# Kernel tuning notes

Measured on AMD Instinct MI355X. Metric: run time of the kernel, lower is better.

## Reference

```python
import jax, jax.numpy as jnp
import numpy as np

V = 6890          # SMPL vertex count
RAYS, POINTS = 256, 64
LATENT_DIM = 16
RES_HI, RES_LO = 10, 4


def posenc(x, res):
    # NeRF-style encoding: [x, sin(2^k x), cos(2^k x)] for k in 0..res-1 -> D*(1+2*res)
    freqs = 2.0 ** jnp.arange(res, dtype=x.dtype)            # [res]
    xf = x[..., None, :] * freqs[:, None]                    # [..., res, D]
    n = x.shape[:-1]
    s = jnp.sin(xf).reshape(*n, -1)
    c = jnp.cos(xf).reshape(*n, -1)
    return jnp.concatenate([x, s, c], axis=-1)


def setup_inputs() -> dict:
    key = jax.random.key(0)
    ks = jax.random.split(key, 12)
    inp = {}
    inp['pts'] = jax.random.normal(ks[0], (RAYS, POINTS, 6), jnp.float32)
    inp['keypoints'] = jax.random.normal(ks[1], (V, 3), jnp.float32)
    # invertible per-vertex 4x4 transforms: identity + small noise, stored [4,4,V]
    noise = 0.1 * jax.random.normal(ks[2], (4, 4, V), jnp.float32)
    inp['trans_kp'] = jnp.eye(4, dtype=jnp.float32)[:, :, None] + noise
    inp['neighbors'] = jax.random.randint(ks[3], (V, 7), 0, V, jnp.int32)
    inp['rest_pose'] = jax.random.normal(ks[4], (V, 3), jnp.float32)
    inp['latent'] = jax.random.normal(ks[5], (V, LATENT_DIM), jnp.float32)
    d_in = 7 * ((2 * RES_HI + 1) * 4 + LATENT_DIM)  # 700
    inp['W1'] = 0.05 * jax.random.normal(ks[6], (d_in, 256), jnp.float32)
    inp['b1'] = jnp.zeros((256,), jnp.float32)
    inp['W2'] = 0.05 * jax.random.normal(ks[7], (256, 256), jnp.float32)
    inp['b2'] = jnp.zeros((256,), jnp.float32)
    inp['W3'] = 0.05 * jax.random.normal(ks[8], (256, 256), jnp.float32)
    inp['b3'] = jnp.zeros((256,), jnp.float32)
    return inp


def reference(pts, keypoints, trans_kp, neighbors, rest_pose, latent,
              W1, b1, W2, b2, W3, b3):
    rays, points, _ = pts.shape
    p, view_dir = jnp.split(pts, 2, axis=-1)
    p = p.reshape(rays * points, 3)                          # [N,3]

    # brute-force 1-NN of p into keypoints
    d2 = ((p * p).sum(-1, keepdims=True)
          - 2.0 * p @ keypoints.T
          + (keypoints * keypoints).sum(-1))                 # [N,V]
    knn_index = jnp.argmin(d2, axis=1)                       # [N]

    # inverse transforms, keep rotation part: [3,3,V]
    T = jnp.linalg.inv(jnp.transpose(trans_kp, (2, 0, 1)))   # [V,4,4]
    R = jnp.transpose(T, (1, 2, 0))[:3, :3]                  # [3,3,V]

    vidx = neighbors[knn_index]                              # [N,7]
    vdist = p[:, None, :] - keypoints[vidx]                  # [N,7,3]

    diff = p - keypoints[knn_index]                          # [N,3]
    Rg = R[:, :, knn_index]                                  # [3,3,N]
    direction = jnp.einsum('ijn,nj->ni', Rg, diff)           # [N,3]
    nrm = jnp.linalg.norm(direction, axis=-1, keepdims=True)
    direction = direction / jnp.maximum(nrm, 1e-12)

    vfeat = jnp.concatenate(
        [rest_pose[vidx].reshape(-1, 21),
         jnp.linalg.norm(vdist, axis=-1)], axis=-1)          # [N,28]
    lfeat = latent[vidx].reshape(-1, 7 * latent.shape[1])    # [N,112]

    h = jnp.concatenate([posenc(vfeat, RES_HI), lfeat], -1)  # [N,700]
    h = jax.nn.relu(h @ W1 + b1)
    h = jax.nn.relu(h @ W2 + b2)
    h = h @ W3 + b3                                          # [N,256]

    out = jnp.concatenate([h, posenc(direction, RES_LO)], -1)  # [N,283]
    return out.reshape(rays, points, -1)
```

## Files before the change

### kernel.cpp

```cpp
#include <hip/hip_runtime.h>
#include <hip/hip_bf16.h>
#include <math.h>

#define V_N   6890
#define N_PTS 16384
#define D_IN  700
#define D_INP 704
#define D_HID 256
#define D_OUT 283
#define NCHUNK 32
#define CHUNK  216
#define GAP_EPS 1e-4f

#define RINV4_OFF 0
#define KP4_OFF   82688
#define RP4_OFF   110272
#define PB4_OFF   170640
#define WT1_OFF   2267792
#define WT2_OFF   2357904
#define WT3_OFF   2390672
#define X_OFF     2423440

typedef __attribute__((ext_vector_type(8))) short short8;
typedef __attribute__((ext_vector_type(4))) float f32x4;

__device__ __forceinline__ unsigned short f2bf(float f) {
    unsigned int u = __builtin_bit_cast(unsigned int, f);
    u += 0x7fffu + ((u >> 16) & 1u);
    return (unsigned short)(u >> 16);
}

__device__ __forceinline__ float fsin(float x) {
    return __builtin_amdgcn_sinf(__builtin_amdgcn_fractf(x * 0.15915494309189535f));
}
__device__ __forceinline__ float fcos(float x) {
    return __builtin_amdgcn_cosf(__builtin_amdgcn_fractf(x * 0.15915494309189535f));
}

__device__ __forceinline__ void glds16(const void* g, void* l) {
    __builtin_amdgcn_global_load_lds(
        (const __attribute__((address_space(1))) void*)g,
        (__attribute__((address_space(3))) void*)l, 16, 0, 0);
}

__device__ __forceinline__ int swzoff(int r, int sub) {
    return ((r << 2) | (sub ^ ((r >> 1) & 3))) << 4;
}

#define SCAN_BLOCKS 2048
#define PREP_BLOCKS 27
__global__ __launch_bounds__(256) void prep_scan_kernel(
    const float* __restrict__ pts, const float* __restrict__ keyp,
    const float* __restrict__ trans, const float* __restrict__ restp,
    const float* __restrict__ W1, const float* __restrict__ W2,
    const float* __restrict__ W3,
    float4* __restrict__ rinv4, float4* __restrict__ kp4, float4* __restrict__ rp4,
    unsigned short* __restrict__ wt1, unsigned short* __restrict__ wt2,
    unsigned short* __restrict__ wt3, float4* __restrict__ pb4)
{
    __shared__ float4 s_kp[CHUNK];
    int bx = blockIdx.x, tid = threadIdx.x;

    if (bx < SCAN_BLOCKS) {
        int c = bx >> 6;
        int n = (bx & 63) * 256 + tid;
        int v0 = c * CHUNK;
        int nv = min(V_N - v0, CHUNK);
        if (tid < nv) {
            int v = v0 + tid;
            float kx = keyp[v*3+0], ky = keyp[v*3+1], kz = keyp[v*3+2];
            s_kp[tid] = make_float4(kx, ky, kz, kx*kx + ky*ky + kz*kz);
        }
        __syncthreads();

        float px2 = 2.0f * pts[n*6+0], py2 = 2.0f * pts[n*6+1], pz2 = 2.0f * pts[n*6+2];
        float m1 = 1e30f, m2 = 1e30f;
        int bi = 0x7fffffff;

#define KNN_STEP(kk, jj)                                            \
    {                                                               \
        float d = kk.w - (px2*kk.x + py2*kk.y + pz2*kk.z);          \
        bool lt = d < m1;                                           \
        m2 = lt ? m1 : fminf(m2, d);                                \
        bi = lt ? (jj) : bi;                                        \
        m1 = fminf(m1, d);                                          \
    }
        int j = 0;
        for (; j + 4 <= nv; j += 4) {
            float4 k0 = s_kp[j], k1 = s_kp[j+1], k2 = s_kp[j+2], k3 = s_kp[j+3];
            KNN_STEP(k0, v0+j); KNN_STEP(k1, v0+j+1);
            KNN_STEP(k2, v0+j+2); KNN_STEP(k3, v0+j+3);
        }
        for (; j < nv; ++j) {
            float4 k0 = s_kp[j];
            KNN_STEP(k0, v0+j);
        }
#undef KNN_STEP
        pb4[(size_t)c*N_PTS + n] = make_float4(m1, m2, __int_as_float(bi), 0.0f);

    } else if (bx < SCAN_BLOCKS + PREP_BLOCKS) {
        int v = (bx - SCAN_BLOCKS) * 256 + tid;
        if (v >= V_N) return;
        float m[16];
#pragma unroll
        for (int i = 0; i < 16; ++i) m[i] = trans[i * V_N + v];

        float i0  =  m[5]*m[10]*m[15] - m[5]*m[11]*m[14] - m[9]*m[6]*m[15] + m[9]*m[7]*m[14] + m[13]*m[6]*m[11] - m[13]*m[7]*m[10];
        float i4  = -m[4]*m[10]*m[15] + m[4]*m[11]*m[14] + m[8]*m[6]*m[15] - m[8]*m[7]*m[14] - m[12]*m[6]*m[11] + m[12]*m[7]*m[10];
        float i8  =  m[4]*m[9]*m[15]  - m[4]*m[11]*m[13] - m[8]*m[5]*m[15] + m[8]*m[7]*m[13] + m[12]*m[5]*m[11] - m[12]*m[7]*m[9];
        float i12 = -m[4]*m[9]*m[14]  + m[4]*m[10]*m[13] + m[8]*m[5]*m[14] - m[8]*m[6]*m[13] - m[12]*m[5]*m[10] + m[12]*m[6]*m[9];
        float i1  = -m[1]*m[10]*m[15] + m[1]*m[11]*m[14] + m[9]*m[2]*m[15] - m[9]*m[3]*m[14] - m[13]*m[2]*m[11] + m[13]*m[3]*m[10];
        float i5  =  m[0]*m[10]*m[15] - m[0]*m[11]*m[14] - m[8]*m[2]*m[15] + m[8]*m[3]*m[14] + m[12]*m[2]*m[11] - m[12]*m[3]*m[10];
        float i9  = -m[0]*m[9]*m[15]  + m[0]*m[11]*m[13] + m[8]*m[1]*m[15] - m[8]*m[3]*m[13] - m[12]*m[1]*m[11] + m[12]*m[3]*m[9];
        float i2  =  m[1]*m[6]*m[15]  - m[1]*m[7]*m[14]  - m[5]*m[2]*m[15] + m[5]*m[3]*m[14] + m[13]*m[2]*m[7]  - m[13]*m[3]*m[6];
        float i6  = -m[0]*m[6]*m[15]  + m[0]*m[7]*m[14]  + m[4]*m[2]*m[15] - m[4]*m[3]*m[14] - m[12]*m[2]*m[7]  + m[12]*m[3]*m[6];
        float i10 =  m[0]*m[5]*m[15]  - m[0]*m[7]*m[13]  - m[4]*m[1]*m[15] + m[4]*m[3]*m[13] + m[12]*m[1]*m[7]  - m[12]*m[3]*m[5];

        float det = m[0]*i0 + m[1]*i4 + m[2]*i8 + m[3]*i12;
        float id = 1.0f / det;
        rinv4[v*3+0] = make_float4(i0*id, i1*id, i2*id, i4*id);
        rinv4[v*3+1] = make_float4(i5*id, i6*id, i8*id, i9*id);
        rinv4[v*3+2] = make_float4(i10*id, 0.0f, 0.0f, 0.0f);

        float kx = keyp[v*3], ky = keyp[v*3+1], kz = keyp[v*3+2];
        kp4[v] = make_float4(kx, ky, kz, kx*kx + ky*ky + kz*kz);
        rp4[v] = make_float4(restp[v*3], restp[v*3+1], restp[v*3+2], 0.0f);
    } else {
        int idx = (bx - SCAN_BLOCKS - PREP_BLOCKS) * 256 + tid;
        const int N1 = 256 * D_INP;
        const int N2 = 256 * 256;
        if (idx < N1) {
            int n = idx / D_INP, k = idx - n * D_INP;
            float v = (k < D_IN) ? W1[k * 256 + n] : 0.0f;
            wt1[n * D_INP + k] = f2bf(v);
        } else if (idx < N1 + N2) {
            int t = idx - N1;
            int n = t >> 8, k = t & 255;
            wt2[n * 256 + k] = f2bf(W2[k * 256 + n]);
        } else if (idx < N1 + 2 * N2) {
            int t = idx - N1 - N2;
            int n = t >> 8, k = t & 255;
            wt3[n * 256 + k] = f2bf(W3[k * 256 + n]);
        }
    }
}

__global__ __launch_bounds__(256) void feat_kernel(
    const float* __restrict__ pts, const int* __restrict__ neigh,
    const float* __restrict__ latent, const float4* __restrict__ rinv4,
    const float4* __restrict__ kp4, const float4* __restrict__ rp4,
    const float4* __restrict__ pb4, unsigned short* __restrict__ X,
    float* __restrict__ out)
{
    __shared__ float s_vf[4][2][29];
    __shared__ float s_dir[4][2][4];

    int t = threadIdx.x;
    int w = t >> 6, lane = t & 63;
    int n0 = blockIdx.x * 8 + w * 2;

    int pl = lane & 1, g = lane >> 1;
    float4 A = pb4[(size_t)g * N_PTS + (n0 + pl)];
    float m1 = A.x, m2 = A.y;
    int   bi = __float_as_int(A.z);
#pragma unroll
    for (int off = 2; off <= 32; off <<= 1) {
        float om1 = __shfl_xor(m1, off);
        float om2 = __shfl_xor(m2, off);
        int   obi = __shfl_xor(bi, off);
        float nm2 = fminf(fminf(m2, om2), fmaxf(m1, om1));
        bool take = (om1 < m1) || (om1 == m1 && obi < bi);
        bi = take ? obi : bi;
        m1 = fminf(m1, om1);
        m2 = nm2;
    }
    bool amb = (m2 - m1 < GAP_EPS);
    unsigned long long mask = __ballot(amb) & 0x3ull;
    while (mask) {
        int src = __ffsll(mask) - 1;
        mask &= mask - 1;
        int nn = n0 + src;
        double pxd = (double)pts[nn*6+0], pyd = (double)pts[nn*6+1], pzd = (double)pts[nn*6+2];
        double ppd = pxd*pxd + pyd*pyd + pzd*pzd;
        double best = 1e300; int bbi = 0x7fffffff;
        for (int jj = lane; jj < V_N; jj += 64) {
            float4 k = kp4[jj];
            double kx = (double)k.x, ky = (double)k.y, kz = (double)k.z;
            double d = ppd - 2.0*(pxd*kx + pyd*ky + pzd*kz) + (kx*kx + ky*ky + kz*kz);
            if (d < best || (d == best && jj < bbi)) { best = d; bbi = jj; }
        }
#pragma unroll
        for (int off = 32; off >= 1; off >>= 1) {
            double od = __shfl_xor(best, off);
            int    oi = __shfl_xor(bbi, off);
            if (od < best || (od == best && oi < bbi)) { best = od; bbi = oi; }
        }
        if (lane == src) bi = bbi;
    }

    int p = lane >> 5, j = lane & 31;
    int np = n0 + p;
    int k8 = __shfl(bi, p);
    float px = pts[np*6+0], py = pts[np*6+1], pz = pts[np*6+2];

    int v7 = 0;
    if (j < 7) {
        v7 = neigh[k8*7 + j];
        float4 kq = kp4[v7];
        float4 rq = rp4[v7];
        float dx = px - kq.x, dy = py - kq.y, dz = pz - kq.z;
        s_vf[w][p][j*3+0] = rq.x;
        s_vf[w][p][j*3+1] = rq.y;
        s_vf[w][p][j*3+2] = rq.z;
        s_vf[w][p][21+j]  = sqrtf(dx*dx + dy*dy + dz*dz);
    } else if (j == 7) {
        float4 kq = kp4[k8];
        float ddx = px - kq.x, ddy = py - kq.y, ddz = pz - kq.z;
        float4 R0 = rinv4[k8*3+0];
        float4 R1 = rinv4[k8*3+1];
        float4 R2 = rinv4[k8*3+2];
        float d0 = R0.x*ddx + R0.y*ddy + R0.z*ddz;
        float d1 = R0.w*ddx + R1.x*ddy + R1.y*ddz;
        float d2 = R1.z*ddx + R1.w*ddy + R2.x*ddz;
        float nrm = fmaxf(sqrtf(d0*d0 + d1*d1 + d2*d2), 1e-12f);
        s_dir[w][p][0] = d0/nrm; s_dir[w][p][1] = d1/nrm; s_dir[w][p][2] = d2/nrm;
    }

#pragma unroll
    for (int pp = 0; pp < 2; ++pp) {
        int n = n0 + pp;
        float dir0 = s_dir[w][pp][0];
        float dir1 = s_dir[w][pp][1];
        float dir2 = s_dir[w][pp][2];

        if (lane < 27) {
            float val;
            if (lane < 3) {
                val = (lane == 0) ? dir0 : (lane == 1) ? dir1 : dir2;
            } else {
                int tt = (lane < 15) ? lane - 3 : lane - 15;
                int m = tt % 3;
                float db = (m == 0) ? dir0 : (m == 1) ? dir1 : dir2;
                float a = db * (float)(1 << (tt/3));
                val = (lane < 15) ? fsin(a) : fcos(a);
            }
            out[(size_t)n*D_OUT + 256 + lane] = val;
        }

#pragma unroll
        for (int it = 0; it < 3; ++it) {
            int base = it * 256 + (lane << 2);
            bool in_range = base < D_INP;
            int region = (base < 28) ? 0 : (base < 308) ? 1 : (base < 588) ? 2
                       : (base < 700) ? 3 : 4;

            int t0 = (region == 1) ? base - 28 : (region == 2) ? base - 308 : 0;
            int q = t0 / 28;
            int r = t0 - q * 28;
            float f0 = (float)(1 << q);
            float a[4];
#pragma unroll
            for (int jj = 0; jj < 4; ++jj) {
                int rj; float fj;
                if (region == 0) { rj = base + jj; fj = 1.0f; }
                else if (region <= 2) {
                    rj = r + jj; fj = f0;
                    if (rj >= 28) { rj -= 28; fj = f0 * 2.0f; }
                } else { rj = 0; fj = 0.0f; }
                a[jj] = s_vf[w][pp][rj] * fj;
            }
            int idxc = (region == 3) ? (base - 588) >> 4 : 0;
            int vL = __shfl(v7, pp*32 + idxc);

            unsigned short r0, r1, r2, r3;
            if (region == 0) {
                r0 = f2bf(a[0]); r1 = f2bf(a[1]); r2 = f2bf(a[2]); r3 = f2bf(a[3]);
            } else if (region == 1) {
                r0 = f2bf(fsin(a[0])); r1 = f2bf(fsin(a[1]));
                r2 = f2bf(fsin(a[2])); r3 = f2bf(fsin(a[3]));
            } else if (region == 2) {
                r0 = f2bf(fcos(a[0])); r1 = f2bf(fcos(a[1]));
                r2 = f2bf(fcos(a[2])); r3 = f2bf(fcos(a[3]));
            } else if (region == 3) {
                int t3 = base - 588;
                float4 lv = *(const float4*)&latent[vL * 16 + (t3 & 15)];
                r0 = f2bf(lv.x); r1 = f2bf(lv.y); r2 = f2bf(lv.z); r3 = f2bf(lv.w);
            } else {
                r0 = r1 = r2 = r3 = 0;
            }
            if (in_range)
                *(ushort4*)&X[(size_t)n * D_INP + base] = make_ushort4(r0, r1, r2, r3);
        }
    }
}

#define HLD 264
__global__ __launch_bounds__(512) void mlp_kernel(
    const unsigned short* __restrict__ X,
    const unsigned short* __restrict__ wt1,
    const unsigned short* __restrict__ wt2,
    const unsigned short* __restrict__ wt3,
    const float* __restrict__ b1, const float* __restrict__ b2,
    const float* __restrict__ b3, float* __restrict__ out)
{
    __shared__ unsigned short As[64 * 32];
    __shared__ unsigned short Ws[256 * 32];
    __shared__ unsigned short H1[64 * HLD];
    __shared__ unsigned short H2[64 * HLD];

    int t = threadIdx.x, l = t & 63, w = t >> 6;
    int bm = blockIdx.x * 64;
    int mbase = (w >> 2) * 32, nbase = (w & 3) * 64;
    int lrow = l & 15, lk = (l >> 4) * 8, sub = l >> 4;
    int col0 = l & 15, rquad = (l >> 4) * 4;

    f32x4 acc[2][4];
    short8 af[2], bf[4];

#pragma unroll
    for (int mi = 0; mi < 2; ++mi)
#pragma unroll
        for (int ni = 0; ni < 4; ++ni) acc[mi][ni] = {0.f, 0.f, 0.f, 0.f};

    for (int k0 = 0; k0 < D_INP; k0 += 32) {
        if (t < 256) {
            int r = t >> 2;
            int sg = (t & 3) ^ ((r >> 1) & 3);
            glds16(X + (size_t)(bm + r) * D_INP + k0 + sg * 8, (char*)As + t * 16);
        }
#pragma unroll
        for (int i = 0; i < 2; ++i) {
            int c = i * 512 + t;
            int r = c >> 2;
            int sg = (c & 3) ^ ((r >> 1) & 3);
            glds16(wt1 + (size_t)r * D_INP + k0 + sg * 8, (char*)Ws + (size_t)c * 16);
        }
        __syncthreads();
#pragma unroll
        for (int mi = 0; mi < 2; ++mi)
            af[mi] = *(const short8*)((const char*)As + swzoff(mbase + mi*16 + lrow, sub));
#pragma unroll
        for (int ni = 0; ni < 4; ++ni)
            bf[ni] = *(const short8*)((const char*)Ws + swzoff(nbase + ni*16 + lrow, sub));
#pragma unroll
        for (int mi = 0; mi < 2; ++mi)
#pragma unroll
            for (int ni = 0; ni < 4; ++ni)
                acc[mi][ni] = __builtin_amdgcn_mfma_f32_16x16x32_bf16(
                    af[mi], bf[ni], acc[mi][ni], 0, 0, 0);
        __syncthreads();
    }
#pragma unroll
    for (int mi = 0; mi < 2; ++mi)
#pragma unroll
        for (int ni = 0; ni < 4; ++ni) {
            int col = nbase + ni * 16 + col0;
            float bv = b1[col];
#pragma unroll
            for (int r = 0; r < 4; ++r) {
                int row = mbase + mi * 16 + rquad + r;
                H1[row * HLD + col] = f2bf(fmaxf(acc[mi][ni][r] + bv, 0.0f));
            }
        }
    __syncthreads();

#pragma unroll
    for (int mi = 0; mi < 2; ++mi)
#pragma unroll
        for (int ni = 0; ni < 4; ++ni) acc[mi][ni] = {0.f, 0.f, 0.f, 0.f};

    for (int k0 = 0; k0 < D_HID; k0 += 32) {
#pragma unroll
        for (int i = 0; i < 2; ++i) {
            int c = i * 512 + t;
            int r = c >> 2;
            int sg = (c & 3) ^ ((r >> 1) & 3);
            glds16(wt2 + (size_t)r * D_HID + k0 + sg * 8, (char*)Ws + (size_t)c * 16);
        }
        __syncthreads();
#pragma unroll
        for (int mi = 0; mi < 2; ++mi)
            af[mi] = *(const short8*)&H1[(mbase + mi * 16 + lrow) * HLD + k0 + lk];
#pragma unroll
        for (int ni = 0; ni < 4; ++ni)
            bf[ni] = *(const short8*)((const char*)Ws + swzoff(nbase + ni*16 + lrow, sub));
#pragma unroll
        for (int mi = 0; mi < 2; ++mi)
#pragma unroll
            for (int ni = 0; ni < 4; ++ni)
                acc[mi][ni] = __builtin_amdgcn_mfma_f32_16x16x32_bf16(
                    af[mi], bf[ni], acc[mi][ni], 0, 0, 0);
        __syncthreads();
    }
#pragma unroll
    for (int mi = 0; mi < 2; ++mi)
#pragma unroll
        for (int ni = 0; ni < 4; ++ni) {
            int col = nbase + ni * 16 + col0;
            float bv = b2[col];
#pragma unroll
            for (int r = 0; r < 4; ++r) {
                int row = mbase + mi * 16 + rquad + r;
                H2[row * HLD + col] = f2bf(fmaxf(acc[mi][ni][r] + bv, 0.0f));
            }
        }
    __syncthreads();

#pragma unroll
    for (int mi = 0; mi < 2; ++mi)
#pragma unroll
        for (int ni = 0; ni < 4; ++ni) acc[mi][ni] = {0.f, 0.f, 0.f, 0.f};

    for (int k0 = 0; k0 < D_HID; k0 += 32) {
#pragma unroll
        for (int i = 0; i < 2; ++i) {
            int c = i * 512 + t;
            int r = c >> 2;
            int sg = (c & 3) ^ ((r >> 1) & 3);
            glds16(wt3 + (size_t)r * D_HID + k0 + sg * 8, (char*)Ws + (size_t)c * 16);
        }
        __syncthreads();
#pragma unroll
        for (int mi = 0; mi < 2; ++mi)
            af[mi] = *(const short8*)&H2[(mbase + mi * 16 + lrow) * HLD + k0 + lk];
#pragma unroll
        for (int ni = 0; ni < 4; ++ni)
            bf[ni] = *(const short8*)((const char*)Ws + swzoff(nbase + ni*16 + lrow, sub));
#pragma unroll
        for (int mi = 0; mi < 2; ++mi)
#pragma unroll
            for (int ni = 0; ni < 4; ++ni)
                acc[mi][ni] = __builtin_amdgcn_mfma_f32_16x16x32_bf16(
                    af[mi], bf[ni], acc[mi][ni], 0, 0, 0);
        __syncthreads();
    }
#pragma unroll
    for (int mi = 0; mi < 2; ++mi)
#pragma unroll
        for (int ni = 0; ni < 4; ++ni) {
            int col = nbase + ni * 16 + col0;
            float bv = b3[col];
#pragma unroll
            for (int r = 0; r < 4; ++r) {
                int row = bm + mbase + mi * 16 + rquad + r;
                out[(size_t)row * D_OUT + col] = acc[mi][ni][r] + bv;
            }
        }
}

extern "C" void kernel_launch(void* const* d_in, const int* in_sizes, int n_in,
                              void* d_out, int out_size, void* d_ws, size_t ws_size,
                              hipStream_t stream) {
    const float* pts    = (const float*)d_in[0];
    const float* keyp   = (const float*)d_in[1];
    const float* trans  = (const float*)d_in[2];
    const int*   neigh  = (const int*)d_in[3];
    const float* restp  = (const float*)d_in[4];
    const float* latent = (const float*)d_in[5];
    const float* W1     = (const float*)d_in[6];
    const float* b1     = (const float*)d_in[7];
    const float* W2     = (const float*)d_in[8];
    const float* b2     = (const float*)d_in[9];
    const float* W3     = (const float*)d_in[10];
    const float* b3     = (const float*)d_in[11];
    float* out = (float*)d_out;

    float* wsf = (float*)d_ws;
    float4*         rinv4 = (float4*)(wsf + RINV4_OFF);
    float4*         kp4   = (float4*)(wsf + KP4_OFF);
    float4*         rp4   = (float4*)(wsf + RP4_OFF);
    float4*         pb4   = (float4*)(wsf + PB4_OFF);
    unsigned short* wt1   = (unsigned short*)(wsf + WT1_OFF);
    unsigned short* wt2   = (unsigned short*)(wsf + WT2_OFF);
    unsigned short* wt3   = (unsigned short*)(wsf + WT3_OFF);
    unsigned short* X     = (unsigned short*)(wsf + X_OFF);

    int wconv_blocks = (256*D_INP + 2*256*256 + 255) / 256;
    prep_scan_kernel<<<SCAN_BLOCKS + PREP_BLOCKS + wconv_blocks, 256, 0, stream>>>(
        pts, keyp, trans, restp, W1, W2, W3, rinv4, kp4, rp4, wt1, wt2, wt3, pb4);
    feat_kernel<<<N_PTS/8, 256, 0, stream>>>(pts, neigh, latent, rinv4,
                                             kp4, rp4, pb4, X, out);
    mlp_kernel<<<N_PTS/64, 512, 0, stream>>>(X, wt1, wt2, wt3, b1, b2, b3, out);
}
```

Baseline: 184.3 us.

## Fuse brute-force KNN scan into feature kernel, dropping chunked partial buffer

The nearest-keypoint search moves out of the prep kernel's 2048 chunked scan blocks and into the feature kernel. Each wave now scans all keypoints for its two points, streaming keypoints from global memory and reducing min and second-min with lane shuffles. This removes the write and re-read of the per-chunk partial results buffer (32 partials per point) and the cross-chunk reduction. In exchange, keypoint loads now come from global memory through the cache rather than being staged in LDS per chunk, and the scan runs as one long serial loop per wave. The double-precision rescan for near-ties is kept, moved into a helper function.

Result: slower. 197.9 us (+7.4%).

```diff
diff --git a/kernel.cpp b/kernel.cpp
--- a/kernel.cpp
+++ b/kernel.cpp
@@ -8,14 +8,11 @@
 #define D_INP 704
 #define D_HID 256
 #define D_OUT 283
-#define NCHUNK 32
-#define CHUNK  216
 #define GAP_EPS 1e-4f
 
 #define RINV4_OFF 0
 #define KP4_OFF   82688
 #define RP4_OFF   110272
-#define PB4_OFF   170640
 #define WT1_OFF   2267792
 #define WT2_OFF   2357904
 #define WT3_OFF   2390672
@@ -47,59 +44,38 @@
     return ((r << 2) | (sub ^ ((r >> 1) & 3))) << 4;
 }
 
-#define SCAN_BLOCKS 2048
+__device__ __forceinline__ int rescan64(const float* __restrict__ pts,
+                                        const float4* __restrict__ kp4,
+                                        int nn, int lane) {
+    double pxd = (double)pts[nn*6+0], pyd = (double)pts[nn*6+1], pzd = (double)pts[nn*6+2];
+    double ppd = pxd*pxd + pyd*pyd + pzd*pzd;
+    double best = 1e300; int bbi = 0x7fffffff;
+    for (int jj = lane; jj < V_N; jj += 64) {
+        float4 k = kp4[jj];
+        double kx = (double)k.x, ky = (double)k.y, kz = (double)k.z;
+        double d = ppd - 2.0*(pxd*kx + pyd*ky + pzd*kz) + (kx*kx + ky*ky + kz*kz);
+        if (d < best || (d == best && jj < bbi)) { best = d; bbi = jj; }
+    }
+#pragma unroll
+    for (int off = 32; off >= 1; off >>= 1) {
+        double od = __shfl_xor(best, off);
+        int    oi = __shfl_xor(bbi, off);
+        if (od < best || (od == best && oi < bbi)) { best = od; bbi = oi; }
+    }
+    return bbi;
+}
+
 #define PREP_BLOCKS 27
-__global__ __launch_bounds__(256) void prep_scan_kernel(
-    const float* __restrict__ pts, const float* __restrict__ keyp,
-    const float* __restrict__ trans, const float* __restrict__ restp,
+__global__ __launch_bounds__(256) void prep_wconv_kernel(
+    const float* __restrict__ trans, const float* __restrict__ keyp,
+    const float* __restrict__ restp,
+    float4* __restrict__ rinv4, float4* __restrict__ kp4, float4* __restrict__ rp4,
     const float* __restrict__ W1, const float* __restrict__ W2,
-    const float* __restrict__ W3,
-    float4* __restrict__ rinv4, float4* __restrict__ kp4, float4* __restrict__ rp4,
-    unsigned short* __restrict__ wt1, unsigned short* __restrict__ wt2,
-    unsigned short* __restrict__ wt3, float4* __restrict__ pb4)
+    const float* __restrict__ W3, unsigned short* __restrict__ wt1,
+    unsigned short* __restrict__ wt2, unsigned short* __restrict__ wt3)
 {
-    __shared__ float4 s_kp[CHUNK];
-    int bx = blockIdx.x, tid = threadIdx.x;
-
-    if (bx < SCAN_BLOCKS) {
-        int c = bx >> 6;
-        int n = (bx & 63) * 256 + tid;
-        int v0 = c * CHUNK;
-        int nv = min(V_N - v0, CHUNK);
-        if (tid < nv) {
-            int v = v0 + tid;
-            float kx = keyp[v*3+0], ky = keyp[v*3+1], kz = keyp[v*3+2];
-            s_kp[tid] = make_float4(kx, ky, kz, kx*kx + ky*ky + kz*kz);
-        }
-        __syncthreads();
-
-        float px2 = 2.0f * pts[n*6+0], py2 = 2.0f * pts[n*6+1], pz2 = 2.0f * pts[n*6+2];
-        float m1 = 1e30f, m2 = 1e30f;
-        int bi = 0x7fffffff;
-
-#define KNN_STEP(kk, jj)                                            \
-    {                                                               \
-        float d = kk.w - (px2*kk.x + py2*kk.y + pz2*kk.z);          \
-        bool lt = d < m1;                                           \
-        m2 = lt ? m1 : fminf(m2, d);                                \
-        bi = lt ? (jj) : bi;                                        \
-        m1 = fminf(m1, d);                                          \
-    }
-        int j = 0;
-        for (; j + 4 <= nv; j += 4) {
-            float4 k0 = s_kp[j], k1 = s_kp[j+1], k2 = s_kp[j+2], k3 = s_kp[j+3];
-            KNN_STEP(k0, v0+j); KNN_STEP(k1, v0+j+1);
-            KNN_STEP(k2, v0+j+2); KNN_STEP(k3, v0+j+3);
-        }
-        for (; j < nv; ++j) {
-            float4 k0 = s_kp[j];
-            KNN_STEP(k0, v0+j);
-        }
-#undef KNN_STEP
-        pb4[(size_t)c*N_PTS + n] = make_float4(m1, m2, __int_as_float(bi), 0.0f);
-
-    } else if (bx < SCAN_BLOCKS + PREP_BLOCKS) {
-        int v = (bx - SCAN_BLOCKS) * 256 + tid;
+    if (blockIdx.x < PREP_BLOCKS) {
+        int v = blockIdx.x * 256 + threadIdx.x;
         if (v >= V_N) return;
         float m[16];
 #pragma unroll
@@ -126,7 +102,7 @@
         kp4[v] = make_float4(kx, ky, kz, kx*kx + ky*ky + kz*kz);
         rp4[v] = make_float4(restp[v*3], restp[v*3+1], restp[v*3+2], 0.0f);
     } else {
-        int idx = (bx - SCAN_BLOCKS - PREP_BLOCKS) * 256 + tid;
+        int idx = (blockIdx.x - PREP_BLOCKS) * 256 + threadIdx.x;
         const int N1 = 256 * D_INP;
         const int N2 = 256 * 256;
         if (idx < N1) {
@@ -149,8 +125,7 @@
     const float* __restrict__ pts, const int* __restrict__ neigh,
     const float* __restrict__ latent, const float4* __restrict__ rinv4,
     const float4* __restrict__ kp4, const float4* __restrict__ rp4,
-    const float4* __restrict__ pb4, unsigned short* __restrict__ X,
-    float* __restrict__ out)
+    unsigned short* __restrict__ X, float* __restrict__ out)
 {
     __shared__ float s_vf[4][2][29];
     __shared__ float s_dir[4][2][4];
@@ -159,48 +134,47 @@
     int w = t >> 6, lane = t & 63;
     int n0 = blockIdx.x * 8 + w * 2;
 
-    int pl = lane & 1, g = lane >> 1;
-    float4 A = pb4[(size_t)g * N_PTS + (n0 + pl)];
-    float m1 = A.x, m2 = A.y;
-    int   bi = __float_as_int(A.z);
-#pragma unroll
-    for (int off = 2; off <= 32; off <<= 1) {
-        float om1 = __shfl_xor(m1, off);
-        float om2 = __shfl_xor(m2, off);
-        int   obi = __shfl_xor(bi, off);
-        float nm2 = fminf(fminf(m2, om2), fmaxf(m1, om1));
-        bool take = (om1 < m1) || (om1 == m1 && obi < bi);
-        bi = take ? obi : bi;
-        m1 = fminf(m1, om1);
-        m2 = nm2;
-    }
-    bool amb = (m2 - m1 < GAP_EPS);
-    unsigned long long mask = __ballot(amb) & 0x3ull;
-    while (mask) {
-        int src = __ffsll(mask) - 1;
-        mask &= mask - 1;
-        int nn = n0 + src;
-        double pxd = (double)pts[nn*6+0], pyd = (double)pts[nn*6+1], pzd = (double)pts[nn*6+2];
-        double ppd = pxd*pxd + pyd*pyd + pzd*pzd;
-        double best = 1e300; int bbi = 0x7fffffff;
-        for (int jj = lane; jj < V_N; jj += 64) {
-            float4 k = kp4[jj];
-            double kx = (double)k.x, ky = (double)k.y, kz = (double)k.z;
-            double d = ppd - 2.0*(pxd*kx + pyd*ky + pzd*kz) + (kx*kx + ky*ky + kz*kz);
-            if (d < best || (d == best && jj < bbi)) { best = d; bbi = jj; }
-        }
-#pragma unroll
-        for (int off = 32; off >= 1; off >>= 1) {
-            double od = __shfl_xor(best, off);
-            int    oi = __shfl_xor(bbi, off);
-            if (od < best || (od == best && oi < bbi)) { best = od; bbi = oi; }
-        }
-        if (lane == src) bi = bbi;
-    }
+    float pxA2 = 2.0f*pts[n0*6+0],     pyA2 = 2.0f*pts[n0*6+1],     pzA2 = 2.0f*pts[n0*6+2];
+    float pxB2 = 2.0f*pts[(n0+1)*6+0], pyB2 = 2.0f*pts[(n0+1)*6+1], pzB2 = 2.0f*pts[(n0+1)*6+2];
+
+    float m1A = 1e30f, m2A = 1e30f; int biA = 0x7fffffff;
+    float m1B = 1e30f, m2B = 1e30f; int biB = 0x7fffffff;
+
+    for (int j = lane; j < 6912; j += 64) {
+        int jc = min(j, V_N - 1);
+        float4 kk = kp4[jc];
+        float dA = kk.w - (pxA2*kk.x + pyA2*kk.y + pzA2*kk.z);
+        float dB = kk.w - (pxB2*kk.x + pyB2*kk.y + pzB2*kk.z);
+        if (j >= V_N) { dA = 1e30f; dB = 1e30f; }
+        bool ltA = dA < m1A;
+        m2A = ltA ? m1A : fminf(m2A, dA);
+        biA = ltA ? j : biA;
+        m1A = fminf(m1A, dA);
+        bool ltB = dB < m1B;
+        m2B = ltB ? m1B : fminf(m2B, dB);
+        biB = ltB ? j : biB;
+        m1B = fminf(m1B, dB);
+    }
+#pragma unroll
+    for (int off = 1; off <= 32; off <<= 1) {
+        float o1 = __shfl_xor(m1A, off), o2 = __shfl_xor(m2A, off);
+        int   ob = __shfl_xor(biA, off);
+        float nm2 = fminf(fminf(m2A, o2), fmaxf(m1A, o1));
+        bool take = (o1 < m1A) || (o1 == m1A && ob < biA);
+        biA = take ? ob : biA;  m1A = fminf(m1A, o1);  m2A = nm2;
+
+        o1 = __shfl_xor(m1B, off);  o2 = __shfl_xor(m2B, off);
+        ob = __shfl_xor(biB, off);
+        nm2 = fminf(fminf(m2B, o2), fmaxf(m1B, o1));
+        take = (o1 < m1B) || (o1 == m1B && ob < biB);
+        biB = take ? ob : biB;  m1B = fminf(m1B, o1);  m2B = nm2;
+    }
+    if (m2A - m1A < GAP_EPS) biA = rescan64(pts, kp4, n0,     lane);
+    if (m2B - m1B < GAP_EPS) biB = rescan64(pts, kp4, n0 + 1, lane);
 
     int p = lane >> 5, j = lane & 31;
     int np = n0 + p;
-    int k8 = __shfl(bi, p);
+    int k8 = p ? biB : biA;
     float px = pts[np*6+0], py = pts[np*6+1], pz = pts[np*6+2];
 
     int v7 = 0;
@@ -469,16 +443,15 @@
     float4*         rinv4 = (float4*)(wsf + RINV4_OFF);
     float4*         kp4   = (float4*)(wsf + KP4_OFF);
     float4*         rp4   = (float4*)(wsf + RP4_OFF);
-    float4*         pb4   = (float4*)(wsf + PB4_OFF);
     unsigned short* wt1   = (unsigned short*)(wsf + WT1_OFF);
     unsigned short* wt2   = (unsigned short*)(wsf + WT2_OFF);
     unsigned short* wt3   = (unsigned short*)(wsf + WT3_OFF);
     unsigned short* X     = (unsigned short*)(wsf + X_OFF);
 
     int wconv_blocks = (256*D_INP + 2*256*256 + 255) / 256;
-    prep_scan_kernel<<<SCAN_BLOCKS + PREP_BLOCKS + wconv_blocks, 256, 0, stream>>>(
-        pts, keyp, trans, restp, W1, W2, W3, rinv4, kp4, rp4, wt1, wt2, wt3, pb4);
+    prep_wconv_kernel<<<PREP_BLOCKS + wconv_blocks, 256, 0, stream>>>(
+        trans, keyp, restp, rinv4, kp4, rp4, W1, W2, W3, wt1, wt2, wt3);
     feat_kernel<<<N_PTS/8, 256, 0, stream>>>(pts, neigh, latent, rinv4,
-                                             kp4, rp4, pb4, X, out);
+                                             kp4, rp4, X, out);
     mlp_kernel<<<N_PTS/64, 512, 0, stream>>>(X, wt1, wt2, wt3, b1, b2, b3, out);
 }
```
